# Kernel tuning notes

Hardware: AMD Instinct MI355X
Metric: run time of the kernel (lower is better)

The kernel has to match this reference:

```python
import jax, jax.numpy as jnp
import numpy as np

N_NEURON = 1024
N_PEPTIDE = 16
N_GENES = 1
BATCH = 2048
SQ = 32  # int(sqrt(N_NEURON))
DT = 1.0 / 120.0
STATE_SIZE = N_NEURON + N_GENES + N_NEURON + N_NEURON * N_PEPTIDE  # 18433


def setup_inputs() -> dict:
    key = jax.random.key(0)
    ks = jax.random.split(key, 10)
    # structured state: [ablate_mat | pc2 | neuron | peptide]
    ablate_mat = jnp.ones((BATCH, N_NEURON), jnp.float32)
    pc2 = jax.random.uniform(ks[0], (BATCH, N_GENES), jnp.float32)
    neuron = jax.random.normal(ks[1], (BATCH, N_NEURON), jnp.float32)
    peptide = jax.random.uniform(ks[2], (BATCH, N_NEURON * N_PEPTIDE), jnp.float32)
    state = jnp.concatenate([ablate_mat, pc2, neuron, peptide], axis=-1)
    u = jax.random.normal(ks[3], (BATCH, 1), jnp.float32)
    # uniform noise sample used by the exp firing noise; keep strictly < 1
    noise_u = jax.random.uniform(ks[4], (BATCH, N_NEURON), jnp.float32, 1e-6, 1.0 - 1e-6)
    D = jax.random.uniform(ks[5], (N_PEPTIDE,), jnp.float32)
    pep_prod_rate = jax.random.uniform(ks[6], (N_PEPTIDE,), jnp.float32)
    pep_decay_rate = jax.random.uniform(ks[7], (N_PEPTIDE,), jnp.float32)
    pep_action = jax.random.normal(ks[8], (N_PEPTIDE,), jnp.float32)
    synapse_matrix = jax.random.normal(ks[9], (N_NEURON, N_NEURON), jnp.float32) * 0.02
    neuron_decay = jnp.ones((1,), jnp.float32) * 0.5
    input_layer = jax.random.normal(jax.random.fold_in(key, 11), (N_NEURON,), jnp.float32)
    return dict(u=u, state=state, noise_u=noise_u, D=D, pep_prod_rate=pep_prod_rate,
                pep_decay_rate=pep_decay_rate, pep_action=pep_action,
                synapse_matrix=synapse_matrix, neuron_decay=neuron_decay,
                input_layer=input_layer)


def reference(u, state, noise_u, D, pep_prod_rate, pep_decay_rate, pep_action,
              synapse_matrix, neuron_decay, input_layer):
    # func = abs (log_train=False)
    Dp = jnp.abs(D)
    prod_r = jnp.abs(pep_prod_rate)
    decay_r = jnp.abs(pep_decay_rate)
    ndecay = jnp.abs(neuron_decay)

    # unpack state: [ablate | pc2 | neuron | peptide]
    ablate_mat = state[:, :N_NEURON]
    pc2 = state[:, N_NEURON:N_NEURON + N_GENES]
    neuron = state[:, N_NEURON + N_GENES:2 * N_NEURON + N_GENES]
    pep_flat = state[:, 2 * N_NEURON + N_GENES:]
    peptide = pep_flat.reshape(-1, N_NEURON, N_PEPTIDE)

    firing = jax.nn.relu(neuron) * ablate_mat
    neuron = neuron * ablate_mat

    # noisy_fire, noise='exp': firing = -(firing+0.01)*log(1-U)
    firing = -(firing + 0.01) * jnp.log1p(-noise_u)
    firing = jnp.clip(firing, 0.0, 10.0)

    # peptide production / decay
    pep_prod = prod_r * firing[:, :, None]           # (b, n, p)
    pep_decay = decay_r * peptide                    # (b, n, p)

    # wrap-around 2D Laplacian diffusion stencil on (SQ, SQ) grid
    ps = peptide.reshape(-1, SQ, SQ, N_PEPTIDE)
    lap = (jnp.roll(ps, -1, axis=1) + jnp.roll(ps, 1, axis=1)
           + jnp.roll(ps, -1, axis=2) + jnp.roll(ps, 1, axis=2) - 4.0 * ps)
    pep_diffuse = (Dp * lap).reshape(-1, N_NEURON, N_PEPTIDE)

    # neuron dynamics
    d_neuron = jnp.sum(peptide * pep_action, axis=-1) * pc2
    d_neuron = d_neuron + firing @ synapse_matrix
    d_neuron = d_neuron - neuron * ndecay
    d_neuron = d_neuron + input_layer * u            # (b,1)*(n,) broadcast

    d_peptide = (pep_prod - pep_decay + pep_diffuse).reshape(-1, N_NEURON * N_PEPTIDE)
    pep_new = pep_flat + d_peptide * DT
    neuron_new = (neuron + d_neuron * DT) * ablate_mat

    state_new = jnp.concatenate([ablate_mat, pc2, neuron_new, pep_new], axis=-1)
    # return_firing=True
    return firing, state_new
```

## Files before the change

### kernel.cpp

```cpp
#include <hip/hip_runtime.h>
#include <hip/hip_bf16.h>

#define N_NEURON 1024
#define N_PEPTIDE 16
#define N_GENES 1
#define BATCH 2048
#define SQ 32
#define DT_STEP (1.0f/120.0f)
#define S_STRIDE (N_NEURON + N_GENES + N_NEURON + N_NEURON*N_PEPTIDE)

typedef __attribute__((ext_vector_type(8))) short short8;
typedef __attribute__((ext_vector_type(4))) short short4v;
typedef __attribute__((ext_vector_type(4))) float floatx4;
typedef floatx4 floatx4u __attribute__((aligned(4)));

__global__ __launch_bounds__(256) void synT_cast(const float* __restrict__ syn,
                                                 __hip_bfloat16* __restrict__ synT) {
    __shared__ float tile[32][33];
    const int n0 = blockIdx.x * 32;
    const int k0 = blockIdx.y * 32;
    const int tx = threadIdx.x & 31;
    const int ty = threadIdx.x >> 5;
    #pragma unroll
    for (int i = 0; i < 4; ++i)
        tile[ty + i*8][tx] = syn[(long)(k0 + ty + i*8) * N_NEURON + n0 + tx];
    __syncthreads();
    #pragma unroll
    for (int i = 0; i < 4; ++i)
        synT[(long)(n0 + ty + i*8) * N_NEURON + k0 + tx] =
            __float2bfloat16(tile[tx][ty + i*8]);
}

__global__ __launch_bounds__(256) void fused_elem(
    const float* __restrict__ u,
    const float* __restrict__ state,
    const float* __restrict__ noise,
    const float* __restrict__ D,
    const float* __restrict__ prod_g,
    const float* __restrict__ decay_g,
    const float* __restrict__ pact_g,
    const float* __restrict__ ndecay_g,
    const float* __restrict__ inL,
    float* __restrict__ firing_out,
    float* __restrict__ state_new,
    __hip_bfloat16* __restrict__ fbf)
{
    __shared__ float sf[N_NEURON];
    __shared__ float sn[N_NEURON];
    __shared__ float sps[N_NEURON];
    const int b = blockIdx.x;
    const int tid = threadIdx.x;
    const long bS = (long)b * S_STRIDE;
    const float u_b = u[b];
    const float pc2 = state[bS + N_NEURON];
    const float ndecay = fabsf(ndecay_g[0]);

    {
        const int n4 = tid * 4;
        floatx4 ab = *(const floatx4u*)(state + bS + n4);
        floatx4 nr = *(const floatx4u*)(state + bS + N_NEURON + N_GENES + n4);
        floatx4 nz = *(const floatx4*)(noise + (long)b * N_NEURON + n4);
        floatx4 f, nm;
        short4v hb;
        #pragma unroll
        for (int j = 0; j < 4; ++j) {
            nm[j] = nr[j] * ab[j];
            float fr = fmaxf(nr[j], 0.f) * ab[j];
            fr = -(fr + 0.01f) * log1pf(-nz[j]);
            fr = fminf(fmaxf(fr, 0.f), 10.f);
            f[j] = fr;
            __hip_bfloat16 h = __float2bfloat16(fr);
            hb[j] = *reinterpret_cast<short*>(&h);
        }
        *(floatx4*)(firing_out + (long)b * N_NEURON + n4) = f;
        *(short4v*)(fbf + (long)b * N_NEURON + n4) = hb;
        *(floatx4u*)(state_new + bS + n4) = ab;
        *(floatx4*)(sf + n4) = f;
        *(floatx4*)(sn + n4) = nm;
    }
    if (tid == 0) state_new[bS + N_NEURON] = pc2;
    __syncthreads();

    const int pq = tid & 3;
    const int nl = tid >> 2;
    const int p0 = pq * 4;
    floatx4 Dq, prq, deq, paq;
    #pragma unroll
    for (int j = 0; j < 4; ++j) {
        Dq[j]  = fabsf(D[p0 + j]);
        prq[j] = fabsf(prod_g[p0 + j]);
        deq[j] = fabsf(decay_g[p0 + j]);
        paq[j] = pact_g[p0 + j];
    }
    const float* __restrict__ pep = state + bS + 2 * N_NEURON + N_GENES;
    float* __restrict__ pep_new = state_new + bS + 2 * N_NEURON + N_GENES;

    #pragma unroll 2
    for (int it = 0; it < 16; ++it) {
        const int n = it * 64 + nl;
        const int si = n >> 5, sj = n & 31;
        const int iup = ((((si + 31) & 31) * 32 + sj) << 4) + p0;
        const int idn = ((((si + 1) & 31) * 32 + sj) << 4) + p0;
        const int ilf = ((si * 32 + ((sj + 31) & 31)) << 4) + p0;
        const int irt = ((si * 32 + ((sj + 1) & 31)) << 4) + p0;
        const int idx = (n << 4) + p0;
        floatx4 c  = *(const floatx4u*)(pep + idx);
        floatx4 vu = *(const floatx4u*)(pep + iup);
        floatx4 vd = *(const floatx4u*)(pep + idn);
        floatx4 vl = *(const floatx4u*)(pep + ilf);
        floatx4 vr = *(const floatx4u*)(pep + irt);
        const float fn = sf[n];
        floatx4 lap = vu + vd + vl + vr - 4.f * c;
        floatx4 outv = c + DT_STEP * (prq * fn - deq * c + Dq * lap);
        *(floatx4u*)(pep_new + idx) = outv;

        float ps = c[0]*paq[0] + c[1]*paq[1] + c[2]*paq[2] + c[3]*paq[3];
        ps += __shfl_xor(ps, 1);
        ps += __shfl_xor(ps, 2);
        if (pq == 0) sps[n] = ps;
    }
    __syncthreads();

    {
        const int n4 = tid * 4;
        floatx4 ss = *(const floatx4*)(sps + n4);
        floatx4 nm = *(const floatx4*)(sn + n4);
        floatx4 il = *(const floatx4*)(inL + n4);
        floatx4 c0;
        #pragma unroll
        for (int j = 0; j < 4; ++j)
            c0[j] = nm[j] + DT_STEP * (ss[j] * pc2 - nm[j] * ndecay + il[j] * u_b);
        *(floatx4u*)(state_new + bS + N_NEURON + N_GENES + n4) = c0;
    }
}

__device__ __forceinline__ void stage8k(const __hip_bfloat16* __restrict__ gbase,
                                        char* lhalf, int row0, int k0,
                                        int w, int lane)
{
    #pragma unroll
    for (int i = 0; i < 2; ++i) {
        const int ch  = w * 2 + i;
        const int o   = ch * 1024 + lane * 16;
        const int row = o >> 7;
        const int c16 = (o >> 4) & 7;
        const int cl  = c16 ^ (row & 7);
        const __hip_bfloat16* g = gbase + (long)(row0 + row) * 1024 + k0 + cl * 8;
        __builtin_amdgcn_global_load_lds(
            (const __attribute__((address_space(1))) void*)g,
            (__attribute__((address_space(3))) void*)(lhalf + ch * 1024),
            16, 0, 0);
    }
}

__device__ __forceinline__ short8 lds_frag(const char* lhalf, int row, int c16) {
    const int cl = c16 ^ (row & 7);
    return *(const short8*)(lhalf + row * 128 + cl * 16);
}

__global__ __launch_bounds__(256) void gemm_epi(
    const __hip_bfloat16* __restrict__ A,
    const __hip_bfloat16* __restrict__ BT,
    const float* __restrict__ state,
    float* __restrict__ state_new)
{
    __shared__ __align__(16) char lds[2][16384];
    const int tid = threadIdx.x;
    const int w = tid >> 6, lane = tid & 63;
    const int q = lane >> 4, l16 = lane & 15;
    const int m0 = blockIdx.x * 64;
    const int n0 = blockIdx.y * 64;
    const int wm = (w & 1) * 32, wn = (w >> 1) * 32;

    floatx4 acc[2][2] = {};

    stage8k(A,  lds[0],        m0, 0, w, lane);
    stage8k(BT, lds[0] + 8192, n0, 0, w, lane);
    __syncthreads();

    int cur = 0;
    for (int t = 0; t < 16; ++t) {
        if (t < 15) {
            stage8k(A,  lds[cur ^ 1],        m0, (t + 1) * 64, w, lane);
            stage8k(BT, lds[cur ^ 1] + 8192, n0, (t + 1) * 64, w, lane);
        }
        const char* la = lds[cur];
        const char* lb = lds[cur] + 8192;
        #pragma unroll
        for (int kk = 0; kk < 2; ++kk) {
            const int c16 = kk * 4 + q;
            short8 a0 = lds_frag(la, wm + l16,      c16);
            short8 a1 = lds_frag(la, wm + 16 + l16, c16);
            short8 b0 = lds_frag(lb, wn + l16,      c16);
            short8 b1 = lds_frag(lb, wn + 16 + l16, c16);
            acc[0][0] = __builtin_amdgcn_mfma_f32_16x16x32_bf16(a0, b0, acc[0][0], 0, 0, 0);
            acc[0][1] = __builtin_amdgcn_mfma_f32_16x16x32_bf16(a0, b1, acc[0][1], 0, 0, 0);
            acc[1][0] = __builtin_amdgcn_mfma_f32_16x16x32_bf16(a1, b0, acc[1][0], 0, 0, 0);
            acc[1][1] = __builtin_amdgcn_mfma_f32_16x16x32_bf16(a1, b1, acc[1][1], 0, 0, 0);
        }
        if (t < 15) __syncthreads();
        cur ^= 1;
    }

    #pragma unroll
    for (int mi = 0; mi < 2; ++mi)
    #pragma unroll
    for (int ni = 0; ni < 2; ++ni)
    #pragma unroll
    for (int r = 0; r < 4; ++r) {
        const int m = m0 + wm + mi * 16 + q * 4 + r;
        const int n = n0 + wn + ni * 16 + l16;
        const long sidx = (long)m * S_STRIDE;
        const float ab = state[sidx + n];
        const float c0 = state_new[sidx + N_NEURON + N_GENES + n];
        state_new[sidx + N_NEURON + N_GENES + n] = (c0 + DT_STEP * acc[mi][ni][r]) * ab;
    }
}

extern "C" void kernel_launch(void* const* d_in, const int* in_sizes, int n_in,
                              void* d_out, int out_size, void* d_ws, size_t ws_size,
                              hipStream_t stream) {
    const float* u      = (const float*)d_in[0];
    const float* state  = (const float*)d_in[1];
    const float* noise  = (const float*)d_in[2];
    const float* D      = (const float*)d_in[3];
    const float* prod   = (const float*)d_in[4];
    const float* decay  = (const float*)d_in[5];
    const float* pact   = (const float*)d_in[6];
    const float* syn    = (const float*)d_in[7];
    const float* ndec   = (const float*)d_in[8];
    const float* inL    = (const float*)d_in[9];

    float* firing = (float*)d_out;
    float* state_new = firing + (long)BATCH * N_NEURON;

    __hip_bfloat16* fbf  = (__hip_bfloat16*)d_ws;
    __hip_bfloat16* synT = fbf + (long)BATCH * N_NEURON;

    hipLaunchKernelGGL(synT_cast, dim3(32, 32), dim3(256), 0, stream, syn, synT);
    hipLaunchKernelGGL(fused_elem, dim3(BATCH), dim3(256), 0, stream,
                       u, state, noise, D, prod, decay, pact, ndec, inL,
                       firing, state_new, fbf);
    hipLaunchKernelGGL(gemm_epi, dim3(32, 16), dim3(256), 0, stream,
                       fbf, synT, state, state_new);
}
```

Measured before the change: 338.0 us.

## Stage peptide stencil slab in LDS with halo rows, split batch rows across two blocks

```diff
diff --git a/kernel.cpp b/kernel.cpp
--- a/kernel.cpp
+++ b/kernel.cpp
@@ -10,9 +10,10 @@
 #define S_STRIDE (N_NEURON + N_GENES + N_NEURON + N_NEURON*N_PEPTIDE)
 
 typedef __attribute__((ext_vector_type(8))) short short8;
-typedef __attribute__((ext_vector_type(4))) short short4v;
 typedef __attribute__((ext_vector_type(4))) float floatx4;
+typedef __attribute__((ext_vector_type(2))) float floatx2;
 typedef floatx4 floatx4u __attribute__((aligned(4)));
+typedef floatx2 floatx2u __attribute__((aligned(4)));
 
 __global__ __launch_bounds__(256) void synT_cast(const float* __restrict__ syn,
                                                  __hip_bfloat16* __restrict__ synT) {
@@ -31,7 +32,7 @@
             __float2bfloat16(tile[tx][ty + i*8]);
 }
 
-__global__ __launch_bounds__(256) void fused_elem(
+__global__ __launch_bounds__(256) void pep_fused(
     const float* __restrict__ u,
     const float* __restrict__ state,
     const float* __restrict__ noise,
@@ -45,92 +46,113 @@
     float* __restrict__ state_new,
     __hip_bfloat16* __restrict__ fbf)
 {
-    __shared__ float sf[N_NEURON];
-    __shared__ float sn[N_NEURON];
-    __shared__ float sps[N_NEURON];
-    const int b = blockIdx.x;
+    __shared__ floatx4 slab4[18 * 128];
+    __shared__ float sf[512];
+    __shared__ float sn[512];
+    __shared__ float sps[512];
+
+    const int b   = blockIdx.x >> 1;
+    const int h   = blockIdx.x & 1;
     const int tid = threadIdx.x;
     const long bS = (long)b * S_STRIDE;
-    const float u_b = u[b];
-    const float pc2 = state[bS + N_NEURON];
+    const int r0  = h * 16;
+    const float u_b  = u[b];
+    const float pc2  = state[bS + N_NEURON];
     const float ndecay = fabsf(ndecay_g[0]);
 
+    const float* __restrict__ pep = state + bS + 2 * N_NEURON + N_GENES;
+    float* __restrict__ pep_new = state_new + bS + 2 * N_NEURON + N_GENES;
+
+    floatx4 sl[8];
+    #pragma unroll
+    for (int k = 0; k < 8; ++k)
+        sl[k] = *(const floatx4u*)(pep + r0 * 512 + (tid + k * 256) * 4);
+    floatx4 halo;
     {
-        const int n4 = tid * 4;
-        floatx4 ab = *(const floatx4u*)(state + bS + n4);
-        floatx4 nr = *(const floatx4u*)(state + bS + N_NEURON + N_GENES + n4);
-        floatx4 nz = *(const floatx4*)(noise + (long)b * N_NEURON + n4);
-        floatx4 f, nm;
-        short4v hb;
+        const int hr = (tid < 128) ? ((r0 + 31) & 31) : ((r0 + 16) & 31);
+        const int ht = tid & 127;
+        halo = *(const floatx4u*)(pep + hr * 512 + ht * 4);
+    }
+
+    const int gn = h * 512 + tid * 2;
+    floatx2 abv = *(const floatx2u*)(state + bS + gn);
+    floatx2 nrv = *(const floatx2u*)(state + bS + N_NEURON + N_GENES + gn);
+    floatx2 nzv = *(const floatx2*)(noise + (long)b * N_NEURON + gn);
+
+    #pragma unroll
+    for (int k = 0; k < 8; ++k)
+        slab4[128 + tid + k * 256] = sl[k];
+    if (tid < 128) slab4[tid] = halo;
+    else           slab4[2176 + tid - 128] = halo;
+
+    {
+        floatx2 fv, nmv;
         #pragma unroll
-        for (int j = 0; j < 4; ++j) {
-            nm[j] = nr[j] * ab[j];
-            float fr = fmaxf(nr[j], 0.f) * ab[j];
-            fr = -(fr + 0.01f) * log1pf(-nz[j]);
+        for (int j = 0; j < 2; ++j) {
+            nmv[j] = nrv[j] * abv[j];
+            float fr = fmaxf(nrv[j], 0.f) * abv[j];
+            fr = -(fr + 0.01f) * log1pf(-nzv[j]);
             fr = fminf(fmaxf(fr, 0.f), 10.f);
-            f[j] = fr;
-            __hip_bfloat16 h = __float2bfloat16(fr);
-            hb[j] = *reinterpret_cast<short*>(&h);
+            fv[j] = fr;
         }
-        *(floatx4*)(firing_out + (long)b * N_NEURON + n4) = f;
-        *(short4v*)(fbf + (long)b * N_NEURON + n4) = hb;
-        *(floatx4u*)(state_new + bS + n4) = ab;
-        *(floatx4*)(sf + n4) = f;
-        *(floatx4*)(sn + n4) = nm;
-    }
-    if (tid == 0) state_new[bS + N_NEURON] = pc2;
+        *(floatx2*)(firing_out + (long)b * N_NEURON + gn) = fv;
+        __hip_bfloat16 h0 = __float2bfloat16(fv[0]);
+        __hip_bfloat16 h1 = __float2bfloat16(fv[1]);
+        unsigned int packed = (unsigned int)(*(unsigned short*)&h0) |
+                              ((unsigned int)(*(unsigned short*)&h1) << 16);
+        *(unsigned int*)(fbf + (long)b * N_NEURON + gn) = packed;
+        *(floatx2u*)(state_new + bS + gn) = abv;
+        *(floatx2*)(sf + tid * 2) = fv;
+        *(floatx2*)(sn + tid * 2) = nmv;
+    }
+    if (h == 0 && tid == 0) state_new[bS + N_NEURON] = pc2;
     __syncthreads();
 
     const int pq = tid & 3;
     const int nl = tid >> 2;
-    const int p0 = pq * 4;
+    const int p0q = pq * 4;
     floatx4 Dq, prq, deq, paq;
     #pragma unroll
     for (int j = 0; j < 4; ++j) {
-        Dq[j]  = fabsf(D[p0 + j]);
-        prq[j] = fabsf(prod_g[p0 + j]);
-        deq[j] = fabsf(decay_g[p0 + j]);
-        paq[j] = pact_g[p0 + j];
-    }
-    const float* __restrict__ pep = state + bS + 2 * N_NEURON + N_GENES;
-    float* __restrict__ pep_new = state_new + bS + 2 * N_NEURON + N_GENES;
+        Dq[j]  = fabsf(D[p0q + j]);
+        prq[j] = fabsf(prod_g[p0q + j]);
+        deq[j] = fabsf(decay_g[p0q + j]);
+        paq[j] = pact_g[p0q + j];
+    }
 
     #pragma unroll 2
-    for (int it = 0; it < 16; ++it) {
-        const int n = it * 64 + nl;
-        const int si = n >> 5, sj = n & 31;
-        const int iup = ((((si + 31) & 31) * 32 + sj) << 4) + p0;
-        const int idn = ((((si + 1) & 31) * 32 + sj) << 4) + p0;
-        const int ilf = ((si * 32 + ((sj + 31) & 31)) << 4) + p0;
-        const int irt = ((si * 32 + ((sj + 1) & 31)) << 4) + p0;
-        const int idx = (n << 4) + p0;
-        floatx4 c  = *(const floatx4u*)(pep + idx);
-        floatx4 vu = *(const floatx4u*)(pep + iup);
-        floatx4 vd = *(const floatx4u*)(pep + idn);
-        floatx4 vl = *(const floatx4u*)(pep + ilf);
-        floatx4 vr = *(const floatx4u*)(pep + irt);
-        const float fn = sf[n];
+    for (int it = 0; it < 8; ++it) {
+        const int n_l  = it * 64 + nl;
+        const int si_l = (n_l >> 5) + 1;
+        const int sj   = n_l & 31;
+        const floatx4 c  = slab4[(si_l * 32 + sj) * 4 + pq];
+        const floatx4 vu = slab4[((si_l - 1) * 32 + sj) * 4 + pq];
+        const floatx4 vd = slab4[((si_l + 1) * 32 + sj) * 4 + pq];
+        const floatx4 vl = slab4[(si_l * 32 + ((sj + 31) & 31)) * 4 + pq];
+        const floatx4 vr = slab4[(si_l * 32 + ((sj + 1) & 31)) * 4 + pq];
+        const float fn = sf[n_l];
         floatx4 lap = vu + vd + vl + vr - 4.f * c;
         floatx4 outv = c + DT_STEP * (prq * fn - deq * c + Dq * lap);
-        *(floatx4u*)(pep_new + idx) = outv;
+        *(floatx4u*)(pep_new + ((h * 512 + n_l) << 4) + p0q) = outv;
 
         float ps = c[0]*paq[0] + c[1]*paq[1] + c[2]*paq[2] + c[3]*paq[3];
         ps += __shfl_xor(ps, 1);
         ps += __shfl_xor(ps, 2);
-        if (pq == 0) sps[n] = ps;
+        if (pq == 0) sps[n_l] = ps;
     }
     __syncthreads();
 
     {
-        const int n4 = tid * 4;
-        floatx4 ss = *(const floatx4*)(sps + n4);
-        floatx4 nm = *(const floatx4*)(sn + n4);
-        floatx4 il = *(const floatx4*)(inL + n4);
-        floatx4 c0;
+        const int n2  = tid * 2;
+        const int gn2 = h * 512 + n2;
+        floatx2 ss = *(const floatx2*)(sps + n2);
+        floatx2 nm = *(const floatx2*)(sn + n2);
+        floatx2 il = *(const floatx2*)(inL + gn2);
+        floatx2 c0;
         #pragma unroll
-        for (int j = 0; j < 4; ++j)
+        for (int j = 0; j < 2; ++j)
             c0[j] = nm[j] + DT_STEP * (ss[j] * pc2 - nm[j] * ndecay + il[j] * u_b);
-        *(floatx4u*)(state_new + bS + N_NEURON + N_GENES + n4) = c0;
+        *(floatx2u*)(state_new + bS + N_NEURON + N_GENES + gn2) = c0;
     }
 }
 
@@ -172,36 +194,7 @@
     const int n0 = blockIdx.y * 64;
     const int wm = (w & 1) * 32, wn = (w >> 1) * 32;
 
-    floatx4 acc[2][2] = {};
-
-    stage8k(A,  lds[0],        m0, 0, w, lane);
-    stage8k(BT, lds[0] + 8192, n0, 0, w, lane);
-    __syncthreads();
-
-    int cur = 0;
-    for (int t = 0; t < 16; ++t) {
-        if (t < 15) {
-            stage8k(A,  lds[cur ^ 1],        m0, (t + 1) * 64, w, lane);
-            stage8k(BT, lds[cur ^ 1] + 8192, n0, (t + 1) * 64, w, lane);
-        }
-        const char* la = lds[cur];
-        const char* lb = lds[cur] + 8192;
-        #pragma unroll
-        for (int kk = 0; kk < 2; ++kk) {
-            const int c16 = kk * 4 + q;
-            short8 a0 = lds_frag(la, wm + l16,      c16);
-            short8 a1 = lds_frag(la, wm + 16 + l16, c16);
-            short8 b0 = lds_frag(lb, wn + l16,      c16);
-            short8 b1 = lds_frag(lb, wn + 16 + l16, c16);
-            acc[0][0] = __builtin_amdgcn_mfma_f32_16x16x32_bf16(a0, b0, acc[0][0], 0, 0, 0);
-            acc[0][1] = __builtin_amdgcn_mfma_f32_16x16x32_bf16(a0, b1, acc[0][1], 0, 0, 0);
-            acc[1][0] = __builtin_amdgcn_mfma_f32_16x16x32_bf16(a1, b0, acc[1][0], 0, 0, 0);
-            acc[1][1] = __builtin_amdgcn_mfma_f32_16x16x32_bf16(a1, b1, acc[1][1], 0, 0, 0);
-        }
-        if (t < 15) __syncthreads();
-        cur ^= 1;
-    }
-
+    float abv[2][2][4], c0v[2][2][4];
     #pragma unroll
     for (int mi = 0; mi < 2; ++mi)
     #pragma unroll
@@ -211,9 +204,57 @@
         const int m = m0 + wm + mi * 16 + q * 4 + r;
         const int n = n0 + wn + ni * 16 + l16;
         const long sidx = (long)m * S_STRIDE;
-        const float ab = state[sidx + n];
-        const float c0 = state_new[sidx + N_NEURON + N_GENES + n];
-        state_new[sidx + N_NEURON + N_GENES + n] = (c0 + DT_STEP * acc[mi][ni][r]) * ab;
+        abv[mi][ni][r] = state[sidx + n];
+        c0v[mi][ni][r] = state_new[sidx + N_NEURON + N_GENES + n];
+    }
+
+    floatx4 acc[2][2] = {};
+
+    stage8k(A,  lds[0],        m0, 0, w, lane);
+    stage8k(BT, lds[0] + 8192, n0, 0, w, lane);
+    __syncthreads();
+
+#define GEMM_STEP(CUR, T)                                                     \
+    {                                                                         \
+        if ((T) < 15) {                                                       \
+            stage8k(A,  lds[(CUR) ^ 1],        m0, ((T) + 1) * 64, w, lane);  \
+            stage8k(BT, lds[(CUR) ^ 1] + 8192, n0, ((T) + 1) * 64, w, lane);  \
+        }                                                                     \
+        const char* la = lds[(CUR)];                                          \
+        const char* lb = lds[(CUR)] + 8192;                                   \
+        _Pragma("unroll")                                                     \
+        for (int kk = 0; kk < 2; ++kk) {                                      \
+            const int c16 = kk * 4 + q;                                       \
+            short8 a0 = lds_frag(la, wm + l16,      c16);                     \
+            short8 a1 = lds_frag(la, wm + 16 + l16, c16);                     \
+            short8 b0 = lds_frag(lb, wn + l16,      c16);                     \
+            short8 b1 = lds_frag(lb, wn + 16 + l16, c16);                     \
+            acc[0][0] = __builtin_amdgcn_mfma_f32_16x16x32_bf16(a0, b0, acc[0][0], 0, 0, 0); \
+            acc[0][1] = __builtin_amdgcn_mfma_f32_16x16x32_bf16(a0, b1, acc[0][1], 0, 0, 0); \
+            acc[1][0] = __builtin_amdgcn_mfma_f32_16x16x32_bf16(a1, b0, acc[1][0], 0, 0, 0); \
+            acc[1][1] = __builtin_amdgcn_mfma_f32_16x16x32_bf16(a1, b1, acc[1][1], 0, 0, 0); \
+        }                                                                     \
+        if ((T) < 15) __syncthreads();                                        \
+    }
+
+    #pragma unroll
+    for (int tt = 0; tt < 8; ++tt) {
+        GEMM_STEP(0, tt * 2)
+        GEMM_STEP(1, tt * 2 + 1)
+    }
+#undef GEMM_STEP
+
+    #pragma unroll
+    for (int mi = 0; mi < 2; ++mi)
+    #pragma unroll
+    for (int ni = 0; ni < 2; ++ni)
+    #pragma unroll
+    for (int r = 0; r < 4; ++r) {
+        const int m = m0 + wm + mi * 16 + q * 4 + r;
+        const int n = n0 + wn + ni * 16 + l16;
+        const long sidx = (long)m * S_STRIDE;
+        state_new[sidx + N_NEURON + N_GENES + n] =
+            (c0v[mi][ni][r] + DT_STEP * acc[mi][ni][r]) * abv[mi][ni][r];
     }
 }
 
@@ -238,7 +279,7 @@
     __hip_bfloat16* synT = fbf + (long)BATCH * N_NEURON;
 
     hipLaunchKernelGGL(synT_cast, dim3(32, 32), dim3(256), 0, stream, syn, synT);
-    hipLaunchKernelGGL(fused_elem, dim3(BATCH), dim3(256), 0, stream,
+    hipLaunchKernelGGL(pep_fused, dim3(BATCH * 2), dim3(256), 0, stream,
                        u, state, noise, D, prod, decay, pact, ndec, inL,
                        firing, state_new, fbf);
     hipLaunchKernelGGL(gemm_epi, dim3(32, 16), dim3(256), 0, stream,
```

Measured after the change: 316.2 us. -6.4%, faster.
